# Kernel tuning notes

Measured on AMD Instinct MI355X. Metric: run time of the kernel, lower is better.

## Reference

```python
import jax, jax.numpy as jnp
import numpy as np

EPS = 1e-12  # torch F.normalize eps


def setup_inputs() -> dict:
    key = jax.random.key(0)
    k1, k2, k3 = jax.random.split(key, 3)
    B, C, N, E, EMB = 128, 16, 128, 4, 16
    OUT = EMB // E  # Linear(emb_sz, emb_sz // num_edges)
    x = jax.random.normal(k1, (B, C, N, EMB), dtype=jnp.float32)
    A = jax.random.uniform(k2, (E, N, N), dtype=jnp.float32)  # non-negative adjacency
    # per-edge-type Linear weights, stored [E, in, out] so y = x @ W[e]
    W = jax.random.normal(k3, (E, EMB, OUT), dtype=jnp.float32) * (1.0 / np.sqrt(EMB))
    return {"x": x, "A": A, "W": W}


def reference(x, A, W):
    # F.normalize(A[e], dim=0): L2-normalize each column -> norm over rows (axis=1 of [E,N,N])
    col_norm = jnp.sqrt(jnp.sum(A * A, axis=1, keepdims=True))  # [E,1,N]
    An = A / jnp.maximum(col_norm, EPS)                         # [E,N,N]
    # x.transpose(3,2) @ An[e] then transpose back:
    # out[e,b,c,m,f] = sum_n x[b,c,n,f] * An[e,n,m]
    msg = jnp.einsum('bcnf,enm->ebcmf', x, An)                  # [E,B,C,N,EMB]
    # per-edge Linear (bias=False) + relu
    h = jax.nn.relu(jnp.einsum('ebcmf,efo->ebcmo', msg, W))     # [E,B,C,N,OUT]
    E_, B, C, N, O = h.shape
    # torch.cat([h_0, h_1, ...], axis=1) -> [B, E*C, N, OUT]
    out = jnp.transpose(h, (1, 0, 2, 3, 4)).reshape(B, E_ * C, N, O)
    return out
```

## Files before the change

kernel.cpp:

```cpp
#include <hip/hip_runtime.h>
#include <math.h>

#define EPSN 1e-12f

typedef __attribute__((ext_vector_type(8))) __bf16 bf16x8;
typedef __attribute__((ext_vector_type(8))) short short8;
typedef __attribute__((ext_vector_type(4))) float floatx4;

static __device__ __forceinline__ unsigned short f2bf(float f) {
    return __builtin_bit_cast(unsigned short, (__bf16)f);
}

__global__ __launch_bounds__(512, 2)
void gcn_one(const float* __restrict__ x, const float* __restrict__ A,
             const float* __restrict__ W, float* __restrict__ out) {
    __shared__ __align__(16) unsigned char xw[32768];
    __shared__ __align__(16) unsigned char at[32768];
    __shared__ float red[4][128];

    const int t   = threadIdx.x;
    const int bc0 = blockIdx.x * 8;
    const int w   = t >> 6;
    const int l   = t & 63;
    const int cl  = l & 15;
    const int lg  = l >> 4;
    const int mw  = w * 16 + cl;
    const int mt  = t & 127;
    const int og  = t >> 7;

    float v[4][8];
    #pragma unroll
    for (int q = 0; q < 4; ++q) {
        int n0 = (og * 4 + q) * 8;
        #pragma unroll
        for (int j = 0; j < 8; ++j)
            v[q][j] = A[(n0 + j) * 128 + mt];
    }

    float4 xf[2][4];
    #pragma unroll
    for (int p = 0; p < 2; ++p) {
        int pair = p * 512 + t;
        int bcl = pair >> 7, n = pair & 127;
        const float4* xp = (const float4*)(x + ((size_t)(bc0 + bcl) * 128 + n) * 16);
        xf[p][0] = xp[0]; xf[p][1] = xp[1]; xf[p][2] = xp[2]; xf[p][3] = xp[3];
    }
    #pragma unroll 1
    for (int e = 0; e < 4; ++e) {
        const float* We = W + e * 64;
        #pragma unroll
        for (int p = 0; p < 2; ++p) {
            int pair = p * 512 + t;
            int bcl = pair >> 7, n = pair & 127;
            float a0 = 0.f, a1 = 0.f, a2 = 0.f, a3 = 0.f;
            #pragma unroll
            for (int f = 0; f < 16; ++f) {
                float xv = ((const float*)&xf[p][f >> 2])[f & 3];
                a0 += xv * We[f * 4 + 0];
                a1 += xv * We[f * 4 + 1];
                a2 += xv * We[f * 4 + 2];
                a3 += xv * We[f * 4 + 3];
            }
            float av[4] = {a0, a1, a2, a3};
            #pragma unroll
            for (int o = 0; o < 4; ++o) {
                int r = bcl * 4 + o;
                int off = (((e * 32 + r) << 8) + n * 2) ^ ((r & 7) << 4);
                *(unsigned short*)(xw + off) = f2bf(av[o]);
            }
        }
    }

    {
        float ssq = 0.f;
        #pragma unroll
        for (int q = 0; q < 4; ++q) {
            int oct = og * 4 + q;
            unsigned short hs[8] __attribute__((aligned(16)));
            #pragma unroll
            for (int j = 0; j < 8; ++j) {
                ssq += v[q][j] * v[q][j];
                hs[j] = f2bf(v[q][j]);
            }
            *(short8*)(at + ((mt << 8) | ((oct ^ (mt & 7)) << 4))) = *(const short8*)hs;
        }
        red[og][mt] = ssq;
    }
    __syncthreads();

    #pragma unroll 1
    for (int e = 0; e < 4; ++e) {
        if (e < 3) {
            const float* An = A + (e + 1) * 16384;
            #pragma unroll
            for (int q = 0; q < 4; ++q) {
                int n0 = (og * 4 + q) * 8;
                #pragma unroll
                for (int j = 0; j < 8; ++j)
                    v[q][j] = An[(n0 + j) * 128 + mt];
            }
        }
        bf16x8 af[2][4];
        #pragma unroll
        for (int rt = 0; rt < 2; ++rt)
            #pragma unroll
            for (int ks = 0; ks < 4; ++ks) {
                int row = rt * 16 + cl;
                int off = (((e * 32 + row) << 8) + (ks * 32 + lg * 8) * 2)
                          ^ ((row & 7) << 4);
                af[rt][ks] = __builtin_bit_cast(bf16x8, *(const short8*)(xw + off));
            }
        bf16x8 bfr[4];
        #pragma unroll
        for (int ks = 0; ks < 4; ++ks) {
            int slot = (ks * 4 + lg) ^ (mw & 7);
            bfr[ks] = __builtin_bit_cast(bf16x8,
                *(const short8*)(at + ((mw << 8) | (slot << 4))));
        }

        floatx4 acc0 = {0.f, 0.f, 0.f, 0.f};
        floatx4 acc1 = {0.f, 0.f, 0.f, 0.f};
        #pragma unroll
        for (int ks = 0; ks < 4; ++ks) {
            acc0 = __builtin_amdgcn_mfma_f32_16x16x32_bf16(af[0][ks], bfr[ks], acc0, 0, 0, 0);
            acc1 = __builtin_amdgcn_mfma_f32_16x16x32_bf16(af[1][ks], bfr[ks], acc1, 0, 0, 0);
        }

        float s = red[0][mw] + red[1][mw] + red[2][mw] + red[3][mw];
        float rn = 1.0f / fmaxf(sqrtf(s), EPSN);

        #pragma unroll
        for (int rt = 0; rt < 2; ++rt) {
            floatx4 a = rt ? acc1 : acc0;
            int bc = bc0 + rt * 4 + lg;
            int b = bc >> 4, c = bc & 15;
            float4 o4;
            o4.x = fmaxf(a[0] * rn, 0.f);
            o4.y = fmaxf(a[1] * rn, 0.f);
            o4.z = fmaxf(a[2] * rn, 0.f);
            o4.w = fmaxf(a[3] * rn, 0.f);
            ((float4*)out)[(size_t)(b * 64 + e * 16 + c) * 128 + mw] = o4;
        }
        __syncthreads();
        if (e < 3) {
            float ssq = 0.f;
            #pragma unroll
            for (int q = 0; q < 4; ++q) {
                int oct = og * 4 + q;
                unsigned short hs[8] __attribute__((aligned(16)));
                #pragma unroll
                for (int j = 0; j < 8; ++j) {
                    ssq += v[q][j] * v[q][j];
                    hs[j] = f2bf(v[q][j]);
                }
                *(short8*)(at + ((mt << 8) | ((oct ^ (mt & 7)) << 4))) =
                    *(const short8*)hs;
            }
            red[og][mt] = ssq;
            __syncthreads();
        }
    }
}

extern "C" void kernel_launch(void* const* d_in, const int* in_sizes, int n_in,
                              void* d_out, int out_size, void* d_ws, size_t ws_size,
                              hipStream_t stream) {
    const float* x = (const float*)d_in[0];
    const float* A = (const float*)d_in[1];
    const float* W = (const float*)d_in[2];
    float* out = (float*)d_out;

    gcn_one<<<256, 512, 0, stream>>>(x, A, W, out);
}
```

Baseline: 19.72 us.

## Compute x@W projection with MFMA and vectorize adjacency loads to float4

The per-edge x·W projection moves from scalar FMAs to a single bf16 MFMA per 16-row tile, with the four edge weight matrices packed into one B fragment. Adjacency loads change from scalar column-strided reads to float4 row reads, with a new thread-to-column mapping, a 16-way partial norm reduction and an adjusted LDS swizzle. This aims to cut VALU work and global load instructions, at the cost of rounding x and W to bf16 before the projection and a longer norm reduction.

```diff
diff --git a/kernel.cpp b/kernel.cpp
--- a/kernel.cpp
+++ b/kernel.cpp
@@ -16,7 +16,7 @@
              const float* __restrict__ W, float* __restrict__ out) {
     __shared__ __align__(16) unsigned char xw[32768];
     __shared__ __align__(16) unsigned char at[32768];
-    __shared__ float red[4][128];
+    __shared__ float red[16][128];
 
     const int t   = threadIdx.x;
     const int bc0 = blockIdx.x * 8;
@@ -25,80 +25,82 @@
     const int cl  = l & 15;
     const int lg  = l >> 4;
     const int mw  = w * 16 + cl;
-    const int mt  = t & 127;
-    const int og  = t >> 7;
+    const int mq  = t & 31;
+    const int ng  = t >> 5;
 
-    float v[4][8];
+    float4 v4[8];
     #pragma unroll
-    for (int q = 0; q < 4; ++q) {
-        int n0 = (og * 4 + q) * 8;
+    for (int j = 0; j < 8; ++j)
+        v4[j] = *(const float4*)(A + (size_t)(ng * 8 + j) * 128 + mq * 4);
+
+    bf16x8 bW;
+    {
+        short8 z = {0, 0, 0, 0, 0, 0, 0, 0};
+        bW = __builtin_bit_cast(bf16x8, z);
+        if (lg < 2) {
+            unsigned short hs[8] __attribute__((aligned(16)));
+            #pragma unroll
+            for (int j = 0; j < 8; ++j)
+                hs[j] = f2bf(W[(cl >> 2) * 64 + (lg * 8 + j) * 4 + (cl & 3)]);
+            bW = __builtin_bit_cast(bf16x8, *(const short8*)hs);
+        }
+    }
+    #pragma unroll
+    for (int ti = 0; ti < 8; ++ti) {
+        int T = w * 8 + ti;
+        bf16x8 ax;
+        { short8 z = {0, 0, 0, 0, 0, 0, 0, 0}; ax = __builtin_bit_cast(bf16x8, z); }
+        if (lg < 2) {
+            int R = T * 16 + cl;
+            const float* xp = x + ((size_t)bc0 * 128 + R) * 16 + lg * 8;
+            float4 a = *(const float4*)xp;
+            float4 b = *(const float4*)(xp + 4);
+            unsigned short hs[8] __attribute__((aligned(16)));
+            hs[0] = f2bf(a.x); hs[1] = f2bf(a.y); hs[2] = f2bf(a.z); hs[3] = f2bf(a.w);
+            hs[4] = f2bf(b.x); hs[5] = f2bf(b.y); hs[6] = f2bf(b.z); hs[7] = f2bf(b.w);
+            ax = __builtin_bit_cast(bf16x8, *(const short8*)hs);
+        }
+        floatx4 d = {0.f, 0.f, 0.f, 0.f};
+        d = __builtin_amdgcn_mfma_f32_16x16x32_bf16(ax, bW, d, 0, 0, 0);
+        int eD = cl >> 2, oD = cl & 3;
+        int bcl = T >> 3;
+        int nb  = (T & 7) * 16 + lg * 4;
+        int r   = bcl * 4 + oD;
+        int base = (eD * 32 + r) << 8;
+        int s    = (r & 7) << 4;
         #pragma unroll
-        for (int j = 0; j < 8; ++j)
-            v[q][j] = A[(n0 + j) * 128 + mt];
-    }
-
-    float4 xf[2][4];
-    #pragma unroll
-    for (int p = 0; p < 2; ++p) {
-        int pair = p * 512 + t;
-        int bcl = pair >> 7, n = pair & 127;
-        const float4* xp = (const float4*)(x + ((size_t)(bc0 + bcl) * 128 + n) * 16);
-        xf[p][0] = xp[0]; xf[p][1] = xp[1]; xf[p][2] = xp[2]; xf[p][3] = xp[3];
-    }
-    #pragma unroll 1
-    for (int e = 0; e < 4; ++e) {
-        const float* We = W + e * 64;
-        #pragma unroll
-        for (int p = 0; p < 2; ++p) {
-            int pair = p * 512 + t;
-            int bcl = pair >> 7, n = pair & 127;
-            float a0 = 0.f, a1 = 0.f, a2 = 0.f, a3 = 0.f;
-            #pragma unroll
-            for (int f = 0; f < 16; ++f) {
-                float xv = ((const float*)&xf[p][f >> 2])[f & 3];
-                a0 += xv * We[f * 4 + 0];
-                a1 += xv * We[f * 4 + 1];
-                a2 += xv * We[f * 4 + 2];
-                a3 += xv * We[f * 4 + 3];
-            }
-            float av[4] = {a0, a1, a2, a3};
-            #pragma unroll
-            for (int o = 0; o < 4; ++o) {
-                int r = bcl * 4 + o;
-                int off = (((e * 32 + r) << 8) + n * 2) ^ ((r & 7) << 4);
-                *(unsigned short*)(xw + off) = f2bf(av[o]);
-            }
+        for (int q = 0; q < 4; ++q) {
+            int off = (base + (nb + q) * 2) ^ s;
+            *(unsigned short*)(xw + off) = f2bf(d[q]);
         }
     }
 
     {
-        float ssq = 0.f;
+        floatx4 rs = {0.f, 0.f, 0.f, 0.f};
         #pragma unroll
-        for (int q = 0; q < 4; ++q) {
-            int oct = og * 4 + q;
+        for (int i = 0; i < 4; ++i) {
+            int m = mq * 4 + i;
             unsigned short hs[8] __attribute__((aligned(16)));
             #pragma unroll
             for (int j = 0; j < 8; ++j) {
-                ssq += v[q][j] * v[q][j];
-                hs[j] = f2bf(v[q][j]);
+                float vv = ((const float*)&v4[j])[i];
+                rs[i] += vv * vv;
+                hs[j] = f2bf(vv);
             }
-            *(short8*)(at + ((mt << 8) | ((oct ^ (mt & 7)) << 4))) = *(const short8*)hs;
+            int slot = ng ^ (mq & 7);
+            *(short8*)(at + ((m << 8) | (slot << 4))) = *(const short8*)hs;
         }
-        red[og][mt] = ssq;
+        *(float4*)&red[ng][mq * 4] = *(const float4*)&rs;
     }
     __syncthreads();
 
     #pragma unroll 1
     for (int e = 0; e < 4; ++e) {
         if (e < 3) {
-            const float* An = A + (e + 1) * 16384;
+            const float* An = A + (size_t)(e + 1) * 16384;
             #pragma unroll
-            for (int q = 0; q < 4; ++q) {
-                int n0 = (og * 4 + q) * 8;
-                #pragma unroll
-                for (int j = 0; j < 8; ++j)
-                    v[q][j] = An[(n0 + j) * 128 + mt];
-            }
+            for (int j = 0; j < 8; ++j)
+                v4[j] = *(const float4*)(An + (size_t)(ng * 8 + j) * 128 + mq * 4);
         }
         bf16x8 af[2][4];
         #pragma unroll
@@ -113,7 +115,7 @@
         bf16x8 bfr[4];
         #pragma unroll
         for (int ks = 0; ks < 4; ++ks) {
-            int slot = (ks * 4 + lg) ^ (mw & 7);
+            int slot = (ks * 4 + lg) ^ ((mw >> 2) & 7);
             bfr[ks] = __builtin_bit_cast(bf16x8,
                 *(const short8*)(at + ((mw << 8) | (slot << 4))));
         }
@@ -126,8 +128,10 @@
             acc1 = __builtin_amdgcn_mfma_f32_16x16x32_bf16(af[1][ks], bfr[ks], acc1, 0, 0, 0);
         }
 
-        float s = red[0][mw] + red[1][mw] + red[2][mw] + red[3][mw];
-        float rn = 1.0f / fmaxf(sqrtf(s), EPSN);
+        float ssum = 0.f;
+        #pragma unroll
+        for (int g = 0; g < 16; ++g) ssum += red[g][mw];
+        float rn = 1.0f / fmaxf(sqrtf(ssum), EPSN);
 
         #pragma unroll
         for (int rt = 0; rt < 2; ++rt) {
@@ -143,20 +147,21 @@
         }
         __syncthreads();
         if (e < 3) {
-            float ssq = 0.f;
+            floatx4 rs = {0.f, 0.f, 0.f, 0.f};
             #pragma unroll
-            for (int q = 0; q < 4; ++q) {
-                int oct = og * 4 + q;
+            for (int i = 0; i < 4; ++i) {
+                int m = mq * 4 + i;
                 unsigned short hs[8] __attribute__((aligned(16)));
                 #pragma unroll
                 for (int j = 0; j < 8; ++j) {
-                    ssq += v[q][j] * v[q][j];
-                    hs[j] = f2bf(v[q][j]);
+                    float vv = ((const float*)&v4[j])[i];
+                    rs[i] += vv * vv;
+                    hs[j] = f2bf(vv);
                 }
-                *(short8*)(at + ((mt << 8) | ((oct ^ (mt & 7)) << 4))) =
-                    *(const short8*)hs;
+                int slot = ng ^ (mq & 7);
+                *(short8*)(at + ((m << 8) | (slot << 4))) = *(const short8*)hs;
             }
-            red[og][mt] = ssq;
+            *(float4*)&red[ng][mq * 4] = *(const float4*)&rs;
             __syncthreads();
         }
     }
```

After: 18.96 us. 1.04x faster.
